# Performance work log

Measured on AMD Instinct MI355X. Metric: run time of the kernel, lower is better.

The kernel has to match this reference:

```python
import jax, jax.numpy as jnp
import numpy as np

INPUT_DIM = 512
OUTPUT_DIM = 32
DEGREE = 8


def setup_inputs() -> dict:
    key = jax.random.key(0)
    kx, kw = jax.random.split(key)
    x = jax.random.normal(kx, (65536, INPUT_DIM), dtype=jnp.float32)
    # xavier_normal_ on [input_dim, output_dim, degree+1]: torch treats last dims as fan;
    # fan_in = output_dim*(degree+1), fan_out = input_dim*(degree+1)
    fan_in = OUTPUT_DIM * (DEGREE + 1)
    fan_out = INPUT_DIM * (DEGREE + 1)
    std = float(np.sqrt(2.0 / (fan_in + fan_out)))
    cheby_coeffs = std * jax.random.normal(kw, (INPUT_DIM, OUTPUT_DIM, DEGREE + 1), dtype=jnp.float32)
    return {"x": x, "cheby_coeffs": cheby_coeffs}


def reference(x, cheby_coeffs):
    xt = jnp.tanh(x.reshape(-1, INPUT_DIM))
    T = [jnp.ones_like(xt), 2.0 * xt]
    for n in range(2, DEGREE + 1):
        T.append(2.0 * xt * T[n - 1] - T[n - 2])
    T = jnp.stack(T, axis=-1)  # [B, I, degree+1]
    y = jnp.einsum('bij,ioj->bo', T, cheby_coeffs)  # [B, O]
    return y
```

## Files before the change

kernel.cpp:

```cpp
#include <hip/hip_runtime.h>
#include <hip/hip_fp16.h>


typedef _Float16 half8 __attribute__((ext_vector_type(8)));
typedef float float4v __attribute__((ext_vector_type(4)));

#define N_ROWS   65536
#define N_I      512
#define N_O      32
#define N_CHUNKS 16
#define STEPS    8
#define CHUNK_F16 8192

__global__ void pack_b(const float* __restrict__ coeffs, _Float16* __restrict__ bsw) {
    int id = blockIdx.x * blockDim.x + threadIdx.x;
    if (id >= 128 * 2 * 64 * 8) return;
    int jj = id & 7;
    int L  = (id >> 3) & 63;
    int t  = (id >> 9) & 1;
    int s  = id >> 10;
    int ci = s >> 3, sl = s & 7;
    int j  = sl + 1;
    int ii = ((L >> 4) << 3) + jj;
    int i  = ci * 32 + ii;
    int o  = t * 16 + (L & 15);
    bsw[id] = (_Float16)coeffs[(i * 32 + o) * 9 + j];
}

__global__ void bias_k(const float* __restrict__ coeffs, float* __restrict__ bias) {
    int o = blockIdx.x;
    int t = threadIdx.x;
    float s = 0.f;
    for (int i = t; i < N_I; i += 64) s += coeffs[(i * 32 + o) * 9 + 0];
    for (int off = 32; off; off >>= 1) s += __shfl_down(s, off, 64);
    if (t == 0) bias[o] = s;
}

__device__ __forceinline__ float fast_tanh(float v) {
    float e = __expf(2.0f * v);
    return __builtin_fmaf(-2.0f, __builtin_amdgcn_rcpf(e + 1.0f), 1.0f);
}

__global__ __launch_bounds__(256, 2) void cheby_main(
        const float* __restrict__ x, const _Float16* __restrict__ bsw,
        const float* __restrict__ bias, float* __restrict__ y) {
    __shared__ __align__(16) _Float16 bl[2][CHUNK_F16];

    const int tid = threadIdx.x;
    const int wv  = tid >> 6;
    const int L   = tid & 63;
    const int q   = L >> 4;
    const int mr  = L & 15;
    const int m0  = blockIdx.x * 128 + wv * 32;
    const int r0  = m0 + mr;
    const int r1  = r0 + 16;

    {
        const uint4* src = (const uint4*)bsw;
        uint4* dst = (uint4*)&bl[0][0];
#pragma unroll
        for (int it = 0; it < 4; ++it) dst[it * 256 + tid] = src[it * 256 + tid];
    }

    float4v acc[2][2];
#pragma unroll
    for (int a = 0; a < 2; ++a)
#pragma unroll
        for (int b = 0; b < 2; ++b)
#pragma unroll
            for (int e = 0; e < 4; ++e) acc[a][b][e] = 0.f;

    for (int ci = 0; ci < N_CHUNKS; ++ci) {
        __syncthreads();
        const int buf = ci & 1;
        if (ci < N_CHUNKS - 1) {
            const uint4* src = (const uint4*)(bsw + (ci + 1) * CHUNK_F16);
            uint4* dst = (uint4*)&bl[buf ^ 1][0];
#pragma unroll
            for (int it = 0; it < 4; ++it) dst[it * 256 + tid] = src[it * 256 + tid];
        }

        const int i0 = ci * 32 + q * 8;
        const float4v xa = *(const float4v*)(x + (size_t)r0 * N_I + i0);
        const float4v xb = *(const float4v*)(x + (size_t)r0 * N_I + i0 + 4);
        const float4v xc = *(const float4v*)(x + (size_t)r1 * N_I + i0);
        const float4v xd = *(const float4v*)(x + (size_t)r1 * N_I + i0 + 4);

        float w0[8], w1[8], up0[8], uc0[8], up1[8], uc1[8];
#pragma unroll
        for (int e = 0; e < 4; ++e) {
            w0[e]     = 2.0f * fast_tanh(xa[e]);
            w0[e + 4] = 2.0f * fast_tanh(xb[e]);
            w1[e]     = 2.0f * fast_tanh(xc[e]);
            w1[e + 4] = 2.0f * fast_tanh(xd[e]);
        }
#pragma unroll
        for (int e = 0; e < 8; ++e) {
            up0[e] = 1.0f; uc0[e] = w0[e];
            up1[e] = 1.0f; uc1[e] = w1[e];
        }

#pragma unroll
        for (int s = 0; s < STEPS; ++s) {
            half8 a0, a1;
#pragma unroll
            for (int e = 0; e < 8; ++e) {
                a0[e] = (_Float16)uc0[e];
                a1[e] = (_Float16)uc1[e];
            }
            const half8 b0 = *(const half8*)&bl[buf][(s * 2 + 0) * 512 + L * 8];
            const half8 b1 = *(const half8*)&bl[buf][(s * 2 + 1) * 512 + L * 8];
            acc[0][0] = __builtin_amdgcn_mfma_f32_16x16x32_f16(a0, b0, acc[0][0], 0, 0, 0);
            acc[0][1] = __builtin_amdgcn_mfma_f32_16x16x32_f16(a0, b1, acc[0][1], 0, 0, 0);
            acc[1][0] = __builtin_amdgcn_mfma_f32_16x16x32_f16(a1, b0, acc[1][0], 0, 0, 0);
            acc[1][1] = __builtin_amdgcn_mfma_f32_16x16x32_f16(a1, b1, acc[1][1], 0, 0, 0);
#pragma unroll
            for (int e = 0; e < 8; ++e) {
                float n0 = __builtin_fmaf(w0[e], uc0[e], -up0[e]);
                float n1 = __builtin_fmaf(w1[e], uc1[e], -up1[e]);
                up0[e] = uc0[e]; uc0[e] = n0;
                up1[e] = uc1[e]; uc1[e] = n1;
            }
        }
    }

    const float b_n0 = bias[mr];
    const float b_n1 = bias[16 + mr];
#pragma unroll
    for (int mt = 0; mt < 2; ++mt) {
#pragma unroll
        for (int e = 0; e < 4; ++e) {
            const int r = m0 + mt * 16 + q * 4 + e;
            y[(size_t)r * N_O + mr]      = acc[mt][0][e] + b_n0;
            y[(size_t)r * N_O + 16 + mr] = acc[mt][1][e] + b_n1;
        }
    }
}

extern "C" void kernel_launch(void* const* d_in, const int* in_sizes, int n_in,
                              void* d_out, int out_size, void* d_ws, size_t ws_size,
                              hipStream_t stream) {
    const float* x      = (const float*)d_in[0];
    const float* coeffs = (const float*)d_in[1];
    float* yout = (float*)d_out;

    _Float16* bsw = (_Float16*)d_ws;
    float* bias   = (float*)((char*)d_ws + 131072 * sizeof(_Float16));

    pack_b<<<512, 256, 0, stream>>>(coeffs, bsw);
    bias_k<<<32, 64, 0, stream>>>(coeffs, bias);
    cheby_main<<<512, 256, 0, stream>>>(x, bsw, bias, yout);
}
```

Baseline: 200.0 us.

## Async LDS copies for coefficients, prefetch x, merge pack and bias kernels

```diff
diff --git a/kernel.cpp b/kernel.cpp
--- a/kernel.cpp
+++ b/kernel.cpp
@@ -12,33 +12,44 @@
 #define STEPS    8
 #define CHUNK_F16 8192
 
-__global__ void pack_b(const float* __restrict__ coeffs, _Float16* __restrict__ bsw) {
-    int id = blockIdx.x * blockDim.x + threadIdx.x;
-    if (id >= 128 * 2 * 64 * 8) return;
-    int jj = id & 7;
-    int L  = (id >> 3) & 63;
-    int t  = (id >> 9) & 1;
-    int s  = id >> 10;
-    int ci = s >> 3, sl = s & 7;
-    int j  = sl + 1;
-    int ii = ((L >> 4) << 3) + jj;
-    int i  = ci * 32 + ii;
-    int o  = t * 16 + (L & 15);
-    bsw[id] = (_Float16)coeffs[(i * 32 + o) * 9 + j];
-}
-
-__global__ void bias_k(const float* __restrict__ coeffs, float* __restrict__ bias) {
-    int o = blockIdx.x;
+__global__ void pack_b_bias(const float* __restrict__ coeffs,
+                            _Float16* __restrict__ bsw,
+                            float* __restrict__ bias) {
+    if (blockIdx.x < 512) {
+        int id = blockIdx.x * 256 + threadIdx.x;
+        int jj = id & 7;
+        int L  = (id >> 3) & 63;
+        int t  = (id >> 9) & 1;
+        int s  = id >> 10;
+        int ci = s >> 3, sl = s & 7;
+        int j  = sl + 1;
+        int ii = ((L >> 4) << 3) + jj;
+        int i  = ci * 32 + ii;
+        int o  = t * 16 + (L & 15);
+        bsw[id] = (_Float16)coeffs[(i * 32 + o) * 9 + j];
+        return;
+    }
     int t = threadIdx.x;
+    int o = t >> 3;
+    int p = t & 7;
     float s = 0.f;
-    for (int i = t; i < N_I; i += 64) s += coeffs[(i * 32 + o) * 9 + 0];
-    for (int off = 32; off; off >>= 1) s += __shfl_down(s, off, 64);
-    if (t == 0) bias[o] = s;
+#pragma unroll
+    for (int k = 0; k < 64; ++k) s += coeffs[((p + k * 8) * 32 + o) * 9 + 0];
+    s += __shfl_xor(s, 4, 64);
+    s += __shfl_xor(s, 2, 64);
+    s += __shfl_xor(s, 1, 64);
+    if (p == 0) bias[o] = s;
 }
 
 __device__ __forceinline__ float fast_tanh(float v) {
     float e = __expf(2.0f * v);
     return __builtin_fmaf(-2.0f, __builtin_amdgcn_rcpf(e + 1.0f), 1.0f);
+}
+
+__device__ __forceinline__ void async_cp16(const _Float16* g, _Float16* l) {
+    typedef const __attribute__((address_space(1))) unsigned int gu32;
+    typedef __attribute__((address_space(3))) unsigned int lu32;
+    __builtin_amdgcn_global_load_lds((gu32*)g, (lu32*)l, 16, 0, 0);
 }
 
 __global__ __launch_bounds__(256, 2) void cheby_main(
@@ -55,12 +66,20 @@
     const int r0  = m0 + mr;
     const int r1  = r0 + 16;
 
+    const float* xrow0 = x + (size_t)r0 * N_I;
+    const float* xrow1 = x + (size_t)r1 * N_I;
+
     {
-        const uint4* src = (const uint4*)bsw;
-        uint4* dst = (uint4*)&bl[0][0];
+        _Float16* dst = &bl[0][0];
 #pragma unroll
-        for (int it = 0; it < 4; ++it) dst[it * 256 + tid] = src[it * 256 + tid];
+        for (int it = 0; it < 4; ++it)
+            async_cp16(bsw + (it * 256 + tid) * 8, dst + (it * 256 + tid) * 8);
     }
+
+    float4v nxa = *(const float4v*)(xrow0 + q * 8);
+    float4v nxb = *(const float4v*)(xrow0 + q * 8 + 4);
+    float4v nxc = *(const float4v*)(xrow1 + q * 8);
+    float4v nxd = *(const float4v*)(xrow1 + q * 8 + 4);
 
     float4v acc[2][2];
 #pragma unroll
@@ -70,21 +89,26 @@
 #pragma unroll
             for (int e = 0; e < 4; ++e) acc[a][b][e] = 0.f;
 
+    __syncthreads();
+
     for (int ci = 0; ci < N_CHUNKS; ++ci) {
-        __syncthreads();
         const int buf = ci & 1;
         if (ci < N_CHUNKS - 1) {
-            const uint4* src = (const uint4*)(bsw + (ci + 1) * CHUNK_F16);
-            uint4* dst = (uint4*)&bl[buf ^ 1][0];
+            const _Float16* src = bsw + (size_t)(ci + 1) * CHUNK_F16;
+            _Float16* dst = &bl[buf ^ 1][0];
 #pragma unroll
-            for (int it = 0; it < 4; ++it) dst[it * 256 + tid] = src[it * 256 + tid];
+            for (int it = 0; it < 4; ++it)
+                async_cp16(src + (it * 256 + tid) * 8, dst + (it * 256 + tid) * 8);
         }
 
-        const int i0 = ci * 32 + q * 8;
-        const float4v xa = *(const float4v*)(x + (size_t)r0 * N_I + i0);
-        const float4v xb = *(const float4v*)(x + (size_t)r0 * N_I + i0 + 4);
-        const float4v xc = *(const float4v*)(x + (size_t)r1 * N_I + i0);
-        const float4v xd = *(const float4v*)(x + (size_t)r1 * N_I + i0 + 4);
+        const float4v xa = nxa, xb = nxb, xc = nxc, xd = nxd;
+        if (ci < N_CHUNKS - 1) {
+            const int i0n = (ci + 1) * 32 + q * 8;
+            nxa = *(const float4v*)(xrow0 + i0n);
+            nxb = *(const float4v*)(xrow0 + i0n + 4);
+            nxc = *(const float4v*)(xrow1 + i0n);
+            nxd = *(const float4v*)(xrow1 + i0n + 4);
+        }
 
         float w0[8], w1[8], up0[8], uc0[8], up1[8], uc1[8];
 #pragma unroll
@@ -122,6 +146,7 @@
                 up1[e] = uc1[e]; uc1[e] = n1;
             }
         }
+        __syncthreads();
     }
 
     const float b_n0 = bias[mr];
@@ -147,7 +172,6 @@
     _Float16* bsw = (_Float16*)d_ws;
     float* bias   = (float*)((char*)d_ws + 131072 * sizeof(_Float16));
 
-    pack_b<<<512, 256, 0, stream>>>(coeffs, bsw);
-    bias_k<<<32, 64, 0, stream>>>(coeffs, bias);
+    pack_b_bias<<<513, 256, 0, stream>>>(coeffs, bsw, bias);
     cheby_main<<<512, 256, 0, stream>>>(x, bsw, bias, yout);
 }
```

Result: slower. 212.7 us (+6.3%).
